# Optimization experiments

Hardware: AMD Instinct MI355X
Metric: run time of the kernel (lower is better)

## Reference

```python
import jax, jax.numpy as jnp
import numpy as np

# Model dims (match init_kwargs / module defaults)
B, D, H, E, K, DEPTH, BS = 8192, 1024, 4096, 16, 2, 2, 64
SP_EXPERT, SP_CROSS = 0.85, 0.9  # block sparsities


def _block_mask(key, n_in, n_out, sparsity):
    """Bool mask [n_in, n_out] with (BS x BS)-block structure, ~(1-sparsity) dense.
    Matches torch.rand(n_blocks_out, n_blocks_in) > sparsity, expanded to full size."""
    mb = jax.random.uniform(key, (n_out // BS, n_in // BS)) > sparsity  # [ob, ib]
    return jnp.repeat(jnp.repeat(mb.T, BS, axis=0), BS, axis=1)  # [n_in, n_out]


def setup_inputs() -> dict:
    key = jax.random.key(0)
    ks = jax.random.split(key, 12)
    x = jax.random.normal(ks[0], (B, D), dtype=jnp.float32)
    gate_w = jax.random.normal(ks[1], (DEPTH, E, D), dtype=jnp.float32) / np.sqrt(D)
    temperature = jnp.ones((DEPTH,), dtype=jnp.float32)
    w1 = jax.random.normal(ks[2], (E, D, H), dtype=jnp.float32) * 0.02
    b1 = jnp.zeros((E, H), dtype=jnp.float32)
    w2 = jax.random.normal(ks[3], (E, H, D), dtype=jnp.float32) * 0.02
    b2 = jnp.zeros((E, D), dtype=jnp.float32)
    cross_w = jax.random.normal(ks[4], (D, D), dtype=jnp.float32) * 0.02
    cross_b = jnp.zeros((D,), dtype=jnp.float32)
    mk = jax.random.split(ks[5], 2 * E + 1)
    mask1 = jnp.stack([_block_mask(mk[i], D, H, SP_EXPERT) for i in range(E)])
    mask2 = jnp.stack([_block_mask(mk[E + i], H, D, SP_EXPERT) for i in range(E)])
    cross_mask = _block_mask(mk[2 * E], D, D, SP_CROSS)
    return {"x": x, "gate_w": gate_w, "temperature": temperature,
            "w1": w1, "b1": b1, "w2": w2, "b2": b2,
            "cross_w": cross_w, "cross_b": cross_b,
            "mask1": mask1, "mask2": mask2, "cross_mask": cross_mask}


def reference(x, gate_w, temperature, w1, b1, w2, b2, cross_w, cross_b,
              mask1, mask2, cross_mask):
    n_tok = x.shape[0]
    # Only the last-depth router affects the output (x is never updated and
    # expert_outputs is re-initialized each depth iteration in the original).
    logits = jnp.einsum('bd,ed->be', x, gate_w[-1]) / temperature[-1]
    top_vals, top_idx = jax.lax.top_k(logits, K)            # [n_tok, K]
    rout_w = jax.nn.softmax(top_vals, axis=-1)
    routing = jnp.zeros((n_tok, E), x.dtype).at[
        jnp.arange(n_tok)[:, None], top_idx].set(rout_w)    # [n_tok, E]

    expert_out = jnp.zeros_like(x)
    for e in range(E):  # fixed small expert count
        h = jax.nn.silu(x @ (w1[e] * mask1[e]) + b1[e])     # [n_tok, H]
        y = h @ (w2[e] * mask2[e]) + b2[e]                  # [n_tok, D]
        expert_out = expert_out + y * routing[:, e:e + 1]
    return x + expert_out @ (cross_w * cross_mask) + cross_b
```

## Files before the change

### kernel.cpp

```cpp
#include <hip/hip_runtime.h>


#define NTOK 8192
#define DIM  1024
#define HID  4096
#define NEXP 16
#define BM   256
#define ROWS_CAP (NTOK*2 + NEXP*256)

typedef __attribute__((ext_vector_type(4))) float fx4;
typedef __attribute__((ext_vector_type(4))) unsigned int ux4;
typedef __attribute__((ext_vector_type(2))) unsigned int ux2;
typedef __attribute__((ext_vector_type(8))) short s8v;
union V16 { ux4 u; s8v s; };

__device__ __forceinline__ unsigned int f2bf(float f) {
  unsigned int u = __float_as_uint(f);
  return (u + 0x7fffu + ((u >> 16) & 1u)) >> 16;
}

__device__ __forceinline__ unsigned int cvt_pk(float lo, float hi) {
  unsigned int r;
  asm("v_cvt_pk_bf16_f32 %0, %1, %2" : "=v"(r) : "v"(lo), "v"(hi));
  return r;
}

__device__ __forceinline__ unsigned int f2fp8(float v) {
  return (unsigned int)__builtin_amdgcn_cvt_pk_fp8_f32(v, v, 0, false) & 0xFFu;
}

__device__ __forceinline__ bool mask_at(const void* m, int flag, size_t idx) {
  if (flag == 0) return ((const unsigned char*)m)[idx] != 0;
  if (flag == 1) return ((const int*)m)[idx] != 0;
  return ((const float*)m)[idx] != 0.0f;
}

__device__ __forceinline__ int flag_of(int ev) {
  return (ev & 2) ? 2 : ((ev & 1) ? 0 : 1);
}

__device__ __forceinline__ int xcd_swz() {
  const int b = blockIdx.x, cpx = gridDim.x >> 3;
  return (b & 7) * cpx + (b >> 3);
}

__global__ void k_route(const float* __restrict__ x,
                        const float* __restrict__ gw,
                        const float* __restrict__ temp,
                        const unsigned int* __restrict__ m1raw,
                        int* __restrict__ top2i, float* __restrict__ top2w,
                        int* __restrict__ meta, unsigned short* __restrict__ xb)
{
  if (blockIdx.x < 64) {
    int bits = 0;
    size_t base = (size_t)blockIdx.x * 4096 + threadIdx.x;
    for (int j = 0; j < 16; j++) {
      unsigned int v = m1raw[base + 256 * j];
      if (v == 0x3f800000u) bits |= 2;
      else if (v > 1u)      bits |= 1;
    }
    if (bits) atomicOr(&meta[1], bits);
  }

  __shared__ float gwsh[NEXP * DIM];
  for (int i = threadIdx.x; i < NEXP * DIM; i += 256) gwsh[i] = gw[i];
  __syncthreads();

  const int wv = threadIdx.x >> 6;
  const int l = threadIdx.x & 63;
  #pragma unroll
  for (int tt = 0; tt < 8; tt++) {
    const int t = blockIdx.x * 32 + wv * 8 + tt;
    const float* xr = x + (size_t)t * DIM;
    float xv[16];
    #pragma unroll
    for (int j = 0; j < 16; j++) xv[j] = xr[l + 64 * j];
    float logit[16];
    #pragma unroll
    for (int e = 0; e < 16; e++) {
      const float* g = gwsh + e * DIM;
      float s = 0.f;
      #pragma unroll
      for (int j = 0; j < 16; j++) s += xv[j] * g[l + 64 * j];
      #pragma unroll
      for (int o = 32; o >= 1; o >>= 1) s += __shfl_xor(s, o);
      logit[e] = s;
    }
    if (l == 0) {
      const float tinv = 1.0f / temp[0];
      int i0 = 0; float v0 = logit[0] * tinv;
      #pragma unroll
      for (int e = 1; e < 16; e++) { float v = logit[e] * tinv; if (v > v0) { v0 = v; i0 = e; } }
      int i1 = -1; float v1 = 0.f; bool first = true;
      #pragma unroll
      for (int e = 0; e < 16; e++) {
        if (e == i0) continue;
        float v = logit[e] * tinv;
        if (first || v > v1) { v1 = v; i1 = e; first = false; }
      }
      float ex = __expf(v1 - v0);
      float den = 1.0f + ex;
      top2i[2 * t] = i0; top2i[2 * t + 1] = i1;
      top2w[2 * t] = 1.0f / den; top2w[2 * t + 1] = ex / den;
      atomicAdd(&meta[8 + i0], 1);
      atomicAdd(&meta[8 + i1], 1);
    }
  }

  {
    const size_t be = (size_t)blockIdx.x * 32 * DIM;
    const fx4* src = (const fx4*)(x + be);
    ux4* dst = (ux4*)(xb + be);
    #pragma unroll
    for (int i = 0; i < 16; i++) {
      const int idx = i * 256 + threadIdx.x;
      fx4 a = src[2 * idx], b = src[2 * idx + 1];
      ux4 o;
      o[0] = cvt_pk(a[0], a[1]);
      o[1] = cvt_pk(a[2], a[3]);
      o[2] = cvt_pk(b[0], b[1]);
      o[3] = cvt_pk(b[2], b[3]);
      dst[idx] = o;
    }
  }
}

__global__ void k_offsets(int* __restrict__ meta) {
  if (threadIdx.x == 0 && blockIdx.x == 0) {
    int o = 0;
    for (int e = 0; e < 16; e++) { meta[32 + e] = o; o += (meta[8 + e] + 255) & ~255; }
    meta[48] = o;
    for (int rt = 0; rt < ROWS_CAP / BM; rt++) {
      const int base = rt * BM;
      int e = 0;
      for (int i = 1; i < 16; i++) if (meta[32 + i] <= base) e = i;
      meta[96 + rt] = e;
    }
  }
}

__global__ void k_assign(const int* __restrict__ top2i,
                         const float* __restrict__ top2w,
                         int* __restrict__ meta, int* __restrict__ tok_of_row,
                         int* __restrict__ t2row)
{
  int t = blockIdx.x * 256 + threadIdx.x;
  if (t >= NTOK) return;
  #pragma unroll
  for (int k = 0; k < 2; k++) {
    int e = top2i[2 * t + k];
    int slot = atomicAdd(&meta[64 + e], 1);
    int row = meta[32 + e] + slot;
    tok_of_row[row] = t;
    t2row[2 * t + k] = row;
  }
}

__global__ __launch_bounds__(256, 2)
void k_gemm1(const unsigned short* __restrict__ xb,
             const float* __restrict__ w1, const float* __restrict__ b1,
             const void* __restrict__ mask1,
             const int* __restrict__ meta, const int* __restrict__ tok_of_row,
             unsigned char* __restrict__ h8)
{
  __shared__ ux4 Ash[2][2048];
  __shared__ __align__(16) ux2 Bsh[2][1024];

  const int bid = xcd_swz();
  const int rt = bid >> 6, ct = bid & 63;
  const int base = rt * BM;
  if (base >= meta[48]) return;
  const int e = meta[96 + rt];

  const int tid = threadIdx.x;
  const int wv = tid >> 6;
  const int jg0 = ct * 64;

  const int l = tid & 63, l16 = l & 15, lhi = l >> 4;
  unsigned int bits;
  {
    const int flag = flag_of(meta[1]);
    bool on = false;
    if (l < 16)
      on = mask_at(mask1, flag, (size_t)e * DIM * HID + (size_t)l * 64 * HID + jg0);
    bits = (unsigned int)(__ballot(on) & 0xFFFFull);
  }

  const unsigned int sseg = (unsigned int)(((tid & 7) ^ ((tid >> 3) & 7)) * 16);
  unsigned int aoff[8];
  #pragma unroll
  for (int i = 0; i < 8; i++) {
    int tok = tok_of_row[base + i * 32 + (tid >> 3)];
    if (tok < 0) tok = 0;
    aoff[i] = (unsigned int)tok * (DIM * 2) + sseg;
  }

  const int kb = tid >> 4, jb = tid & 15;

  fx4 acc[4][4] = {};

  auto STAGE_A = [&](int b, int d0) {
    const char* gp = (const char*)xb + (d0 << 1);
    #pragma unroll
    for (int i = 0; i < 8; i++)
      __builtin_amdgcn_global_load_lds(
        (const __attribute__((address_space(1))) unsigned int*)(gp + aoff[i]),
        (__attribute__((address_space(3))) unsigned int*)&Ash[b][i * 256 + wv * 64],
        16, 0, 0);
  };
  auto LOAD_B = [&](fx4* r, int d0) {
    const float* bp = w1 + ((size_t)e * DIM + d0 + kb * 4) * HID + jg0 + jb * 4;
    r[0] = *(const fx4*)bp;
    r[1] = *(const fx4*)(bp + HID);
    r[2] = *(const fx4*)(bp + 2 * HID);
    r[3] = *(const fx4*)(bp + 3 * HID);
  };
  auto WRITE_B = [&](int b, const fx4* r) {
    #pragma unroll
    for (int jj = 0; jj < 4; jj++) {
      ux2 val;
      val[0] = cvt_pk(r[0][jj], r[1][jj]);
      val[1] = cvt_pk(r[2][jj], r[3][jj]);
      const int col = jb * 4 + jj;
      Bsh[b][(col * 8 + ((kb >> 1) ^ (col & 7))) * 2 + (kb & 1)] = val;
    }
  };
  auto COMPUTE = [&](int b) {
    #pragma unroll
    for (int ks = 0; ks < 2; ks++) {
      s8v a[4], bb[4];
      const int seg = ks * 4 + lhi;
      #pragma unroll
      for (int m = 0; m < 4; m++) {
        const int row = wv * 64 + m * 16 + l16;
        V16 v; v.u = Ash[b][row * 8 + (seg ^ (row & 7))]; a[m] = v.s;
      }
      #pragma unroll
      for (int n = 0; n < 4; n++) {
        const int col = n * 16 + l16;
        V16 v; v.u = ((const ux4*)&Bsh[b][0])[col * 8 + (seg ^ (col & 7))]; bb[n] = v.s;
      }
      #pragma unroll
      for (int m = 0; m < 4; m++)
        #pragma unroll
        for (int n = 0; n < 4; n++)
          acc[m][n] = __builtin_amdgcn_mfma_f32_16x16x32_bf16(a[m], bb[n], acc[m][n], 0, 0, 0);
    }
  };

  if (bits) {
    int d0 = (__ffs(bits) - 1) << 6; bits &= bits - 1;
    {
      fx4 br[4];
      STAGE_A(0, d0);
      LOAD_B(br, d0);
      WRITE_B(0, br);
    }
    __syncthreads();
    int cur = 0;
    for (;;) {
      int nd0 = -1;
      fx4 br2[4];
      if (bits) { nd0 = (__ffs(bits) - 1) << 6; bits &= bits - 1; }
      if (nd0 >= 0) { STAGE_A(cur ^ 1, nd0); LOAD_B(br2, nd0); }
      COMPUTE(cur);
      if (nd0 >= 0) WRITE_B(cur ^ 1, br2);
      __syncthreads();
      cur ^= 1;
      if (nd0 < 0) break;
    }
  }

  unsigned char* hs = (unsigned char*)&Ash[0][0];
  __syncthreads();
  #pragma unroll
  for (int m = 0; m < 4; m++)
    #pragma unroll
    for (int n = 0; n < 4; n++) {
      const int gcol = jg0 + n * 16 + l16;
      const float bbv = b1[e * HID + gcol];
      #pragma unroll
      for (int i = 0; i < 4; i++) {
        const int row = wv * 64 + m * 16 + lhi * 4 + i;
        float v = acc[m][n][i] + bbv;
        float hval = v / (1.0f + __expf(-v));
        hs[row * 64 + n * 16 + l16] = (unsigned char)f2fp8(hval * 8.0f);
      }
    }
  __syncthreads();
  {
    const ux4* s = (const ux4*)hs;
    #pragma unroll
    for (int j = 0; j < 4; j++) {
      const int c2 = j * 256 + tid;
      const int row = c2 >> 2;
      *(ux4*)(h8 + (size_t)(base + row) * HID + ct * 64 + (c2 & 3) * 16) = s[c2];
    }
  }
}

__global__ __launch_bounds__(256, 3)
void k_gemm2(const unsigned char* __restrict__ h8,
             const float* __restrict__ w2, const float* __restrict__ b2,
             const void* __restrict__ mask2,
             const int* __restrict__ meta, unsigned short* __restrict__ yb)
{
  __shared__ ux4 Ash[2][1024];
  __shared__ __align__(16) unsigned int Bsh[2][1024];

  const int bid = xcd_swz();
  const int rt = bid >> 4, ct = bid & 15;
  const int base = rt * BM;
  if (base >= meta[48]) return;
  const int e = meta[96 + rt];

  const int tid = threadIdx.x;
  const int wv = tid >> 6;
  const int jg0 = ct * 64;

  const int l = tid & 63, l16 = l & 15, lhi = l >> 4;
  unsigned long long bits;
  {
    const int flag = flag_of(meta[1]);
    bits = __ballot(mask_at(mask2, flag,
             (size_t)e * HID * DIM + (size_t)l * 64 * DIM + jg0));
  }

  const unsigned int sw = (unsigned int)((tid & 3) ^ ((tid >> 3) & 3));
  unsigned int aoff[4];
  #pragma unroll
  for (int i = 0; i < 4; i++)
    aoff[i] = (unsigned int)(base + i * 64 + (tid >> 2)) * (unsigned int)HID + sw * 16;

  const int kb = tid >> 4, jb = tid & 15;

  fx4 acc[4][4] = {};

  auto STAGE_A = [&](int b, int d0) {
    const char* gp = (const char*)h8 + d0;
    #pragma unroll
    for (int i = 0; i < 4; i++)
      __builtin_amdgcn_global_load_lds(
        (const __attribute__((address_space(1))) unsigned int*)(gp + aoff[i]),
        (__attribute__((address_space(3))) unsigned int*)&Ash[b][i * 256 + wv * 64],
        16, 0, 0);
  };
  auto LOAD_B = [&](fx4* r, int d0) {
    const float* bp = w2 + ((size_t)e * HID + d0 + kb * 4) * DIM + jg0 + jb * 4;
    r[0] = *(const fx4*)bp;
    r[1] = *(const fx4*)(bp + DIM);
    r[2] = *(const fx4*)(bp + 2 * DIM);
    r[3] = *(const fx4*)(bp + 3 * DIM);
  };
  auto WRITE_B = [&](int b, const fx4* r) {
    #pragma unroll
    for (int jj = 0; jj < 4; jj++) {
      const int col = jb * 4 + jj;
      unsigned int u = (unsigned int)__builtin_amdgcn_cvt_pk_fp8_f32(
                          r[0][jj] * 16.0f, r[1][jj] * 16.0f, 0, false);
      u = (unsigned int)__builtin_amdgcn_cvt_pk_fp8_f32(
                          r[2][jj] * 16.0f, r[3][jj] * 16.0f, (int)u, true);
      Bsh[b][col * 16 + (((kb >> 2) ^ ((col >> 1) & 3)) << 2) + (kb & 3)] = u;
    }
  };
  auto COMPUTE = [&](int b) {
    const char* Ab = (const char*)&Ash[b][0];
    const char* Bb = (const char*)&Bsh[b][0];
    #pragma unroll
    for (int ks = 0; ks < 2; ks++) {
      const int c = ks * 2 + (lhi >> 1);
      const int sub = (lhi & 1) << 3;
      long long a[4], bb[4];
      #pragma unroll
      for (int m = 0; m < 4; m++) {
        const int row = wv * 64 + m * 16 + l16;
        a[m] = *(const long long*)(Ab + row * 64 + ((c ^ ((row >> 1) & 3)) << 4) + sub);
      }
      #pragma unroll
      for (int n = 0; n < 4; n++) {
        const int col = n * 16 + l16;
        bb[n] = *(const long long*)(Bb + col * 64 + ((c ^ ((col >> 1) & 3)) << 4) + sub);
      }
      #pragma unroll
      for (int m = 0; m < 4; m++)
        #pragma unroll
        for (int n = 0; n < 4; n++)
          acc[m][n] = __builtin_amdgcn_mfma_f32_16x16x32_fp8_fp8(a[m], bb[n], acc[m][n], 0, 0, 0);
    }
  };

  if (bits) {
    int d0 = (__ffsll(bits) - 1) << 6; bits &= bits - 1;
    {
      fx4 br[4];
      STAGE_A(0, d0);
      LOAD_B(br, d0);
      WRITE_B(0, br);
    }
    __syncthreads();
    int cur = 0;
    for (;;) {
      int nd0 = -1;
      fx4 br2[4];
      if (bits) { nd0 = (__ffsll(bits) - 1) << 6; bits &= bits - 1; }
      if (nd0 >= 0) { STAGE_A(cur ^ 1, nd0); LOAD_B(br2, nd0); }
      COMPUTE(cur);
      if (nd0 >= 0) WRITE_B(cur ^ 1, br2);
      __syncthreads();
      cur ^= 1;
      if (nd0 < 0) break;
    }
  }

  unsigned short* hs = (unsigned short*)&Ash[0][0];
  __syncthreads();
  #pragma unroll
  for (int m = 0; m < 4; m++)
    #pragma unroll
    for (int n = 0; n < 4; n++) {
      const int gcol = jg0 + n * 16 + l16;
      const float bbv = b2[e * DIM + gcol];
      #pragma unroll
      for (int i = 0; i < 4; i++) {
        const int row = wv * 64 + m * 16 + lhi * 4 + i;
        hs[row * 64 + n * 16 + l16] =
            (unsigned short)f2bf(acc[m][n][i] * 0.0078125f + bbv);
      }
    }
  __syncthreads();
  {
    const ux4* s = (const ux4*)hs;
    #pragma unroll
    for (int j = 0; j < 8; j++) {
      const int c2 = j * 256 + tid;
      const int row = c2 >> 3;
      *(ux4*)(yb + (size_t)(base + row) * DIM + ct * 64 + (c2 & 7) * 8) = s[c2];
    }
  }
}

__global__ __launch_bounds__(256, 2)
void k_cross(const unsigned short* __restrict__ yb, const float* __restrict__ x,
             const float* __restrict__ cw, const float* __restrict__ cb,
             const void* __restrict__ cmask, const int* __restrict__ meta,
             const int* __restrict__ t2row, const float* __restrict__ t2w,
             float* __restrict__ out)
{
  __shared__ ux4 Ash[2048];
  __shared__ __align__(16) ux2 Bsh[1024];

  const int bid = xcd_swz();
  const int rt = bid >> 4, ct = bid & 15;
  const int base = rt * BM;
  const int tid = threadIdx.x;
  const int jg0 = ct * 64;

  const int wave = tid >> 6, l = tid & 63;
  const int l16 = l & 15, lhi = l >> 4;

  unsigned int bits;
  {
    const int flag = flag_of(meta[1]);
    bool on = false;
    if (l < 16)
      on = mask_at(cmask, flag, (size_t)l * 64 * DIM + jg0);
    bits = (unsigned int)(__ballot(on) & 0xFFFFull);
  }

  const int tok = base + tid;
  const int r0 = t2row[2 * tok], r1 = t2row[2 * tok + 1];
  const float w0 = t2w[2 * tok], w1 = t2w[2 * tok + 1];

  fx4 acc[4][4] = {};

  while (bits) {
    const int kbx = __ffs(bits) - 1; bits &= bits - 1;
    const int d0 = kbx * 64;
    {
      const ux4* s0 = (const ux4*)(yb + (size_t)r0 * DIM + d0);
      const ux4* s1 = (const ux4*)(yb + (size_t)r1 * DIM + d0);
      #pragma unroll
      for (int seg = 0; seg < 8; seg++) {
        ux4 v0 = s0[seg], v1 = s1[seg], o;
        #pragma unroll
        for (int j = 0; j < 4; j++) {
          float alo = __uint_as_float(v0[j] << 16);
          float ahi = __uint_as_float(v0[j] & 0xFFFF0000u);
          float blo = __uint_as_float(v1[j] << 16);
          float bhi = __uint_as_float(v1[j] & 0xFFFF0000u);
          o[j] = cvt_pk(w0 * alo + w1 * blo, w0 * ahi + w1 * bhi);
        }
        Ash[tid * 8 + (seg ^ (tid & 7))] = o;
      }
    }
    {
      const int kbt = tid >> 4, jb = tid & 15;
      const float* bp = cw + (size_t)(d0 + kbt * 4) * DIM + jg0 + jb * 4;
      fx4 r0v = *(const fx4*)bp;
      fx4 r1v = *(const fx4*)(bp + DIM);
      fx4 r2v = *(const fx4*)(bp + 2 * DIM);
      fx4 r3v = *(const fx4*)(bp + 3 * DIM);
      #pragma unroll
      for (int jj = 0; jj < 4; jj++) {
        ux2 val;
        val[0] = cvt_pk(r0v[jj], r1v[jj]);
        val[1] = cvt_pk(r2v[jj], r3v[jj]);
        const int col = jb * 4 + jj;
        Bsh[(col * 8 + ((kbt >> 1) ^ (col & 7))) * 2 + (kbt & 1)] = val;
      }
    }
    __syncthreads();
    #pragma unroll
    for (int ks = 0; ks < 2; ks++) {
      s8v a[4], b[4];
      const int seg = ks * 4 + lhi;
      #pragma unroll
      for (int m = 0; m < 4; m++) {
        const int row = wave * 64 + m * 16 + l16;
        V16 v; v.u = Ash[row * 8 + (seg ^ (row & 7))]; a[m] = v.s;
      }
      #pragma unroll
      for (int n = 0; n < 4; n++) {
        const int col = n * 16 + l16;
        V16 v; v.u = ((const ux4*)Bsh)[col * 8 + (seg ^ (col & 7))]; b[n] = v.s;
      }
      #pragma unroll
      for (int m = 0; m < 4; m++)
        #pragma unroll
        for (int n = 0; n < 4; n++)
          acc[m][n] = __builtin_amdgcn_mfma_f32_16x16x32_bf16(a[m], b[n], acc[m][n], 0, 0, 0);
    }
    __syncthreads();
  }

  #pragma unroll
  for (int m = 0; m < 4; m++)
    #pragma unroll
    for (int n = 0; n < 4; n++) {
      const int gcol = jg0 + n * 16 + l16;
      #pragma unroll
      for (int i = 0; i < 4; i++) {
        const int lrow = wave * 64 + m * 16 + lhi * 4 + i;
        const size_t idx = (size_t)(base + lrow) * DIM + gcol;
        out[idx] = acc[m][n][i] + x[idx] + cb[gcol];
      }
    }
}

extern "C" void kernel_launch(void* const* d_in, const int* in_sizes, int n_in,
                              void* d_out, int out_size, void* d_ws, size_t ws_size,
                              hipStream_t stream)
{
  (void)in_sizes; (void)n_in; (void)out_size; (void)ws_size;
  const float* x      = (const float*)d_in[0];
  const float* gate_w = (const float*)d_in[1];
  const float* temp   = (const float*)d_in[2];
  const float* w1     = (const float*)d_in[3];
  const float* b1     = (const float*)d_in[4];
  const float* w2     = (const float*)d_in[5];
  const float* b2     = (const float*)d_in[6];
  const float* cw     = (const float*)d_in[7];
  const float* cb     = (const float*)d_in[8];
  const void*  mask1  = d_in[9];
  const void*  mask2  = d_in[10];
  const void*  cmask  = d_in[11];
  float* out = (float*)d_out;
  char* ws = (char*)d_ws;

  size_t off = 0;
  auto walloc = [&](size_t b) { size_t r = off; off = (off + b + 255) & ~(size_t)255; return r; };
  size_t o_meta = walloc(4096);
  size_t o_t2i  = walloc((size_t)NTOK * 2 * 4);
  size_t o_t2w  = walloc((size_t)NTOK * 2 * 4);
  size_t o_t2r  = walloc((size_t)NTOK * 2 * 4);
  size_t o_tok  = walloc((size_t)ROWS_CAP * 4);
  size_t o_xbf  = walloc((size_t)NTOK * DIM * 2);
  size_t o_y    = walloc((size_t)ROWS_CAP * DIM * 2);
  size_t o_hc   = walloc((size_t)ROWS_CAP * HID);

  int*                meta = (int*)(ws + o_meta);
  int*                t2i  = (int*)(ws + o_t2i);
  float*              t2w  = (float*)(ws + o_t2w);
  int*                t2r  = (int*)(ws + o_t2r);
  int*                tok  = (int*)(ws + o_tok);
  unsigned short*     xbf  = (unsigned short*)(ws + o_xbf);
  unsigned short*     yb   = (unsigned short*)(ws + o_y);
  unsigned char*      h8   = (unsigned char*)(ws + o_hc);

  hipMemsetAsync(ws + o_meta, 0, 4096, stream);
  hipMemsetAsync(ws + o_tok, 0xFF, (size_t)ROWS_CAP * 4, stream);

  k_route  <<<NTOK / 32, 256, 0, stream>>>(x, gate_w + (size_t)1 * NEXP * DIM, temp + 1,
                                           (const unsigned int*)mask1, t2i, t2w, meta, xbf);
  k_offsets<<<1, 64, 0, stream>>>(meta);
  k_assign <<<NTOK / 256, 256, 0, stream>>>(t2i, t2w, meta, tok, t2r);

  const int NRT = ROWS_CAP / BM;
  k_gemm1<<<NRT * 64, 256, 0, stream>>>(xbf, w1, b1, mask1, meta, tok, h8);
  k_gemm2<<<NRT * 16, 256, 0, stream>>>(h8, w2, b2, mask2, meta, yb);
  k_cross<<<(NTOK / BM) * 16, 256, 0, stream>>>(yb, x, cw, cb, cmask, meta, t2r, t2w, out);
}
```

Before: 374.7 us.

## Switch expert GEMM1 from bf16 to scaled fp8 MFMA

Converts x to fp8 (scaled by 16) in the routing kernel instead of bf16, converts w1 tiles to fp8 in shared memory, and uses the fp8 16x16x32 MFMA in gemm1 with matching unscaling in the epilogue. This halves A-operand gather traffic and LDS footprint and uses the higher-throughput fp8 MFMA path, at the cost of extra quantisation error on activations and weights. It also replaces the full memset of tok_of_row with a targeted padding fill inside k_offsets, and raises launch bounds occupancy to 3 blocks for gemm1 and cross.

```diff
diff --git a/kernel.cpp b/kernel.cpp
--- a/kernel.cpp
+++ b/kernel.cpp
@@ -29,6 +29,12 @@
   return (unsigned int)__builtin_amdgcn_cvt_pk_fp8_f32(v, v, 0, false) & 0xFFu;
 }
 
+__device__ __forceinline__ unsigned int pk4fp8(float a, float b, float c, float d) {
+  unsigned int u = (unsigned int)__builtin_amdgcn_cvt_pk_fp8_f32(a, b, 0, false);
+  u = (unsigned int)__builtin_amdgcn_cvt_pk_fp8_f32(c, d, (int)u, true);
+  return u;
+}
+
 __device__ __forceinline__ bool mask_at(const void* m, int flag, size_t idx) {
   if (flag == 0) return ((const unsigned char*)m)[idx] != 0;
   if (flag == 1) return ((const int*)m)[idx] != 0;
@@ -49,7 +55,7 @@
                         const float* __restrict__ temp,
                         const unsigned int* __restrict__ m1raw,
                         int* __restrict__ top2i, float* __restrict__ top2w,
-                        int* __restrict__ meta, unsigned short* __restrict__ xb)
+                        int* __restrict__ meta, unsigned char* __restrict__ x8)
 {
   if (blockIdx.x < 64) {
     int bits = 0;
@@ -110,23 +116,24 @@
   {
     const size_t be = (size_t)blockIdx.x * 32 * DIM;
     const fx4* src = (const fx4*)(x + be);
-    ux4* dst = (ux4*)(xb + be);
-    #pragma unroll
-    for (int i = 0; i < 16; i++) {
+    ux4* dst = (ux4*)(x8 + be);
+    #pragma unroll
+    for (int i = 0; i < 8; i++) {
       const int idx = i * 256 + threadIdx.x;
-      fx4 a = src[2 * idx], b = src[2 * idx + 1];
+      fx4 a = src[4 * idx], b = src[4 * idx + 1];
+      fx4 c = src[4 * idx + 2], d = src[4 * idx + 3];
       ux4 o;
-      o[0] = cvt_pk(a[0], a[1]);
-      o[1] = cvt_pk(a[2], a[3]);
-      o[2] = cvt_pk(b[0], b[1]);
-      o[3] = cvt_pk(b[2], b[3]);
+      o[0] = pk4fp8(a[0] * 16.f, a[1] * 16.f, a[2] * 16.f, a[3] * 16.f);
+      o[1] = pk4fp8(b[0] * 16.f, b[1] * 16.f, b[2] * 16.f, b[3] * 16.f);
+      o[2] = pk4fp8(c[0] * 16.f, c[1] * 16.f, c[2] * 16.f, c[3] * 16.f);
+      o[3] = pk4fp8(d[0] * 16.f, d[1] * 16.f, d[2] * 16.f, d[3] * 16.f);
       dst[idx] = o;
     }
   }
 }
 
-__global__ void k_offsets(int* __restrict__ meta) {
-  if (threadIdx.x == 0 && blockIdx.x == 0) {
+__global__ void k_offsets(int* __restrict__ meta, int* __restrict__ tok_of_row) {
+  if (threadIdx.x == 0) {
     int o = 0;
     for (int e = 0; e < 16; e++) { meta[32 + e] = o; o += (meta[8 + e] + 255) & ~255; }
     meta[48] = o;
@@ -136,6 +143,12 @@
       for (int i = 1; i < 16; i++) if (meta[32 + i] <= base) e = i;
       meta[96 + rt] = e;
     }
+  }
+  __syncthreads();
+  const int total = meta[48];
+  for (int r = threadIdx.x; r < total; r += 256) {
+    const int e = meta[96 + r / BM];
+    if (r >= meta[32 + e] + meta[8 + e]) tok_of_row[r] = -1;
   }
 }
 
@@ -156,15 +169,15 @@
   }
 }
 
-__global__ __launch_bounds__(256, 2)
-void k_gemm1(const unsigned short* __restrict__ xb,
+__global__ __launch_bounds__(256, 3)
+void k_gemm1(const unsigned char* __restrict__ x8,
              const float* __restrict__ w1, const float* __restrict__ b1,
              const void* __restrict__ mask1,
              const int* __restrict__ meta, const int* __restrict__ tok_of_row,
              unsigned char* __restrict__ h8)
 {
-  __shared__ ux4 Ash[2][2048];
-  __shared__ __align__(16) ux2 Bsh[2][1024];
+  __shared__ ux4 Ash[2][1024];
+  __shared__ __align__(16) unsigned int Bsh[2][1024];
 
   const int bid = xcd_swz();
   const int rt = bid >> 6, ct = bid & 63;
@@ -175,8 +188,8 @@
   const int tid = threadIdx.x;
   const int wv = tid >> 6;
   const int jg0 = ct * 64;
-
   const int l = tid & 63, l16 = l & 15, lhi = l >> 4;
+
   unsigned int bits;
   {
     const int flag = flag_of(meta[1]);
@@ -186,13 +199,13 @@
     bits = (unsigned int)(__ballot(on) & 0xFFFFull);
   }
 
-  const unsigned int sseg = (unsigned int)(((tid & 7) ^ ((tid >> 3) & 7)) * 16);
-  unsigned int aoff[8];
+  const unsigned int sw = (unsigned int)((tid & 3) ^ ((tid >> 3) & 3));
+  unsigned int aoff[4];
   #pragma unroll
-  for (int i = 0; i < 8; i++) {
-    int tok = tok_of_row[base + i * 32 + (tid >> 3)];
+  for (int i = 0; i < 4; i++) {
+    int tok = tok_of_row[base + i * 64 + (tid >> 2)];
     if (tok < 0) tok = 0;
-    aoff[i] = (unsigned int)tok * (DIM * 2) + sseg;
+    aoff[i] = (unsigned int)tok * (unsigned int)DIM + sw * 16;
   }
 
   const int kb = tid >> 4, jb = tid & 15;
@@ -200,9 +213,9 @@
   fx4 acc[4][4] = {};
 
   auto STAGE_A = [&](int b, int d0) {
-    const char* gp = (const char*)xb + (d0 << 1);
-    #pragma unroll
-    for (int i = 0; i < 8; i++)
+    const char* gp = (const char*)x8 + d0;
+    #pragma unroll
+    for (int i = 0; i < 4; i++)
       __builtin_amdgcn_global_load_lds(
         (const __attribute__((address_space(1))) unsigned int*)(gp + aoff[i]),
         (__attribute__((address_space(3))) unsigned int*)&Ash[b][i * 256 + wv * 64],
@@ -218,33 +231,35 @@
   auto WRITE_B = [&](int b, const fx4* r) {
     #pragma unroll
     for (int jj = 0; jj < 4; jj++) {
-      ux2 val;
-      val[0] = cvt_pk(r[0][jj], r[1][jj]);
-      val[1] = cvt_pk(r[2][jj], r[3][jj]);
       const int col = jb * 4 + jj;
-      Bsh[b][(col * 8 + ((kb >> 1) ^ (col & 7))) * 2 + (kb & 1)] = val;
+      unsigned int u = pk4fp8(r[0][jj] * 16.0f, r[1][jj] * 16.0f,
+                              r[2][jj] * 16.0f, r[3][jj] * 16.0f);
+      Bsh[b][col * 16 + (((kb >> 2) ^ ((col >> 1) & 3)) << 2) + (kb & 3)] = u;
     }
   };
   auto COMPUTE = [&](int b) {
+    const char* Ab = (const char*)&Ash[b][0];
+    const char* Bb = (const char*)&Bsh[b][0];
     #pragma unroll
     for (int ks = 0; ks < 2; ks++) {
-      s8v a[4], bb[4];
-      const int seg = ks * 4 + lhi;
+      const int c = ks * 2 + (lhi >> 1);
+      const int sub = (lhi & 1) << 3;
+      long long a[4], bb[4];
       #pragma unroll
       for (int m = 0; m < 4; m++) {
         const int row = wv * 64 + m * 16 + l16;
-        V16 v; v.u = Ash[b][row * 8 + (seg ^ (row & 7))]; a[m] = v.s;
+        a[m] = *(const long long*)(Ab + row * 64 + ((c ^ ((row >> 1) & 3)) << 4) + sub);
       }
       #pragma unroll
       for (int n = 0; n < 4; n++) {
         const int col = n * 16 + l16;
-        V16 v; v.u = ((const ux4*)&Bsh[b][0])[col * 8 + (seg ^ (col & 7))]; bb[n] = v.s;
+        bb[n] = *(const long long*)(Bb + col * 64 + ((c ^ ((col >> 1) & 3)) << 4) + sub);
       }
       #pragma unroll
       for (int m = 0; m < 4; m++)
         #pragma unroll
         for (int n = 0; n < 4; n++)
-          acc[m][n] = __builtin_amdgcn_mfma_f32_16x16x32_bf16(a[m], bb[n], acc[m][n], 0, 0, 0);
+          acc[m][n] = __builtin_amdgcn_mfma_f32_16x16x32_fp8_fp8(a[m], bb[n], acc[m][n], 0, 0, 0);
     }
   };
 
@@ -282,7 +297,7 @@
       #pragma unroll
       for (int i = 0; i < 4; i++) {
         const int row = wv * 64 + m * 16 + lhi * 4 + i;
-        float v = acc[m][n][i] + bbv;
+        float v = acc[m][n][i] * 0.00390625f + bbv;
         float hval = v / (1.0f + __expf(-v));
         hs[row * 64 + n * 16 + l16] = (unsigned char)f2fp8(hval * 8.0f);
       }
@@ -356,10 +371,8 @@
     #pragma unroll
     for (int jj = 0; jj < 4; jj++) {
       const int col = jb * 4 + jj;
-      unsigned int u = (unsigned int)__builtin_amdgcn_cvt_pk_fp8_f32(
-                          r[0][jj] * 16.0f, r[1][jj] * 16.0f, 0, false);
-      u = (unsigned int)__builtin_amdgcn_cvt_pk_fp8_f32(
-                          r[2][jj] * 16.0f, r[3][jj] * 16.0f, (int)u, true);
+      unsigned int u = pk4fp8(r[0][jj] * 16.0f, r[1][jj] * 16.0f,
+                              r[2][jj] * 16.0f, r[3][jj] * 16.0f);
       Bsh[b][col * 16 + (((kb >> 2) ^ ((col >> 1) & 3)) << 2) + (kb & 3)] = u;
     }
   };
@@ -439,7 +452,7 @@
   }
 }
 
-__global__ __launch_bounds__(256, 2)
+__global__ __launch_bounds__(256, 3)
 void k_cross(const unsigned short* __restrict__ yb, const float* __restrict__ x,
              const float* __restrict__ cw, const float* __restrict__ cb,
              const void* __restrict__ cmask, const int* __restrict__ meta,
@@ -574,7 +587,7 @@
   size_t o_t2w  = walloc((size_t)NTOK * 2 * 4);
   size_t o_t2r  = walloc((size_t)NTOK * 2 * 4);
   size_t o_tok  = walloc((size_t)ROWS_CAP * 4);
-  size_t o_xbf  = walloc((size_t)NTOK * DIM * 2);
+  size_t o_x8   = walloc((size_t)NTOK * DIM);
   size_t o_y    = walloc((size_t)ROWS_CAP * DIM * 2);
   size_t o_hc   = walloc((size_t)ROWS_CAP * HID);
 
@@ -583,20 +596,19 @@
   float*              t2w  = (float*)(ws + o_t2w);
   int*                t2r  = (int*)(ws + o_t2r);
   int*                tok  = (int*)(ws + o_tok);
-  unsigned short*     xbf  = (unsigned short*)(ws + o_xbf);
+  unsigned char*      x8   = (unsigned char*)(ws + o_x8);
   unsigned short*     yb   = (unsigned short*)(ws + o_y);
   unsigned char*      h8   = (unsigned char*)(ws + o_hc);
 
   hipMemsetAsync(ws + o_meta, 0, 4096, stream);
-  hipMemsetAsync(ws + o_tok, 0xFF, (size_t)ROWS_CAP * 4, stream);
 
   k_route  <<<NTOK / 32, 256, 0, stream>>>(x, gate_w + (size_t)1 * NEXP * DIM, temp + 1,
-                                           (const unsigned int*)mask1, t2i, t2w, meta, xbf);
-  k_offsets<<<1, 64, 0, stream>>>(meta);
+                                           (const unsigned int*)mask1, t2i, t2w, meta, x8);
+  k_offsets<<<1, 256, 0, stream>>>(meta, tok);
   k_assign <<<NTOK / 256, 256, 0, stream>>>(t2i, t2w, meta, tok, t2r);
 
   const int NRT = ROWS_CAP / BM;
-  k_gemm1<<<NRT * 64, 256, 0, stream>>>(xbf, w1, b1, mask1, meta, tok, h8);
+  k_gemm1<<<NRT * 64, 256, 0, stream>>>(x8, w1, b1, mask1, meta, tok, h8);
   k_gemm2<<<NRT * 16, 256, 0, stream>>>(h8, w2, b2, mask2, meta, yb);
   k_cross<<<(NTOK / BM) * 16, 256, 0, stream>>>(yb, x, cw, cb, cmask, meta, t2r, t2w, out);
 }
```

After: 351.8 us. 6.1% less time.
